# Kernel tuning notes

Measured on AMD Instinct MI355X. Metric: run time of the kernel, lower is better.

Reference implementation:

```python
import jax, jax.numpy as jnp
import numpy as np

H = 4096        # hidden_size
NH = 32         # num attention heads
HD = 128        # head_dim
NKV = 8         # num kv heads
NREP = NH // NKV
THETA = 1e6     # Mixtral rope_theta
EPS = 1e-5      # rmsnorm eps
NBITS = 4       # kv cache quant bits
GROUP = 128     # kv cache quant group size (== head_dim)


def rms_norm(x, w, eps=EPS):
    var = jnp.mean(x * x, axis=-1, keepdims=True)
    return x * jax.lax.rsqrt(var + eps) * w


def fake_int8_per_token(x):
    # symmetric per-row (per-token) int8 quant-dequant: models QLinear.prepare_input
    s = jnp.maximum(jnp.max(jnp.abs(x), axis=-1, keepdims=True) / 127.0, 1e-8)
    return jnp.clip(jnp.round(x / s), -127, 127) * s


def fake_int8_per_channel(w):
    # symmetric per-output-channel int8 quant-dequant of weight [out, in]
    s = jnp.maximum(jnp.max(jnp.abs(w), axis=-1, keepdims=True) / 127.0, 1e-8)
    return jnp.clip(jnp.round(w / s), -127, 127) * s


def qlinear(x_q, w):
    # x_q already fake-quantized activation; w quantized per-channel
    return jnp.einsum('td,od->to', x_q, fake_int8_per_channel(w))


def quantize_int_group(x, nbits=NBITS, group=GROUP):
    # asymmetric min-max group quant-dequant along last dim
    shp = x.shape
    xg = x.reshape(shp[:-1] + (shp[-1] // group, group))
    mn = jnp.min(xg, axis=-1, keepdims=True)
    mx = jnp.max(xg, axis=-1, keepdims=True)
    scale = jnp.maximum((mx - mn) / (2 ** nbits - 1), 1e-8)
    q = jnp.clip(jnp.round((xg - mn) / scale), 0, 2 ** nbits - 1)
    return (q * scale + mn).reshape(shp)


def rotate_half(x):
    x1, x2 = jnp.split(x, 2, axis=-1)
    return jnp.concatenate((-x2, x1), axis=-1)


def rope_tables(seq_len, dim=HD, theta=THETA):
    inv_freq = 1.0 / (theta ** (jnp.arange(0, dim, 2, dtype=jnp.float32) / dim))
    freqs = jnp.arange(seq_len, dtype=jnp.float32)[:, None] * inv_freq[None, :]
    emb = jnp.concatenate((freqs, freqs), axis=-1)  # [S, HD]
    return jnp.cos(emb), jnp.sin(emb)


def setup_inputs() -> dict:
    key = jax.random.key(0)
    ks = jax.random.split(key, 7)
    B, S = 1, 2048
    return {
        'hidden_states': jax.random.normal(ks[0], (B, S, H), dtype=jnp.float32),
        'position_ids': jnp.broadcast_to(jnp.arange(S, dtype=jnp.int32)[None, :], (B, S)),
        'rmsnorm_weight': jax.random.uniform(ks[1], (H,), dtype=jnp.float32, minval=0.5, maxval=1.5),
        'Wq': jax.random.normal(ks[2], (H, H), dtype=jnp.float32) * 0.02,
        'Wk': jax.random.normal(ks[3], (NKV * HD, H), dtype=jnp.float32) * 0.02,
        'Wv': jax.random.normal(ks[4], (NKV * HD, H), dtype=jnp.float32) * 0.02,
        'Wo': jax.random.normal(ks[5], (H, H), dtype=jnp.float32) * 0.02,
    }


def reference(hidden_states, position_ids, rmsnorm_weight, Wq, Wk, Wv, Wo):
    B, S, _ = hidden_states.shape
    x2d = hidden_states.reshape(B * S, H)

    # fused RMSNorm + activation quant (SHARQ prepare_input_rmsnorm)
    xq = fake_int8_per_token(rms_norm(x2d, rmsnorm_weight))

    q = qlinear(xq, Wq).reshape(B, S, NH, HD).transpose(0, 2, 1, 3)    # [B,NH,S,HD]
    k = qlinear(xq, Wk).reshape(B, S, NKV, HD).transpose(0, 2, 1, 3)   # [B,NKV,S,HD]
    v = qlinear(xq, Wv).reshape(B, S, NKV, HD).transpose(0, 2, 1, 3)

    # int4 group quant of K before RoPE (q_kv_cache=True path)
    k = quantize_int_group(k)

    cos_t, sin_t = rope_tables(S)
    cos = cos_t[position_ids][:, None, :, :]   # [B,1,S,HD]
    sin = sin_t[position_ids][:, None, :, :]
    q = q * cos + rotate_half(q) * sin
    k = k * cos + rotate_half(k) * sin

    # GQA repeat (each kv head repeated NREP times consecutively)
    k = jnp.repeat(k, NREP, axis=1)
    v = jnp.repeat(v, NREP, axis=1)

    # int4 group quant of V after repeat (as in source ordering)
    v = quantize_int_group(v)

    # causal SDPA
    scores = jnp.einsum('bhqd,bhkd->bhqk', q, k) / jnp.sqrt(jnp.float32(HD))
    causal = jnp.tril(jnp.ones((S, S), dtype=bool))
    scores = jnp.where(causal[None, None], scores, jnp.float32(-1e9))
    attn = jax.nn.softmax(scores, axis=-1)
    out = jnp.einsum('bhqk,bhkd->bhqd', attn, v)
    out = out.transpose(0, 2, 1, 3).reshape(B * S, H)

    # o_proj with activation quant
    out = qlinear(fake_int8_per_token(out), Wo)
    return out.reshape(B, S, H)
```

## Files before the change

### kernel.cpp

```cpp
#include <hip/hip_runtime.h>


#define SQ   2048
#define HID  4096
#define NHEAD 32
#define HDIM 128
#define NKVH 8
#define KVD  1024
#define QKVN 6144

typedef __attribute__((ext_vector_type(8))) short          bh8;
typedef __attribute__((ext_vector_type(8))) unsigned short us8;
typedef __attribute__((ext_vector_type(4))) float          f4v;
typedef __attribute__((ext_vector_type(4))) int            i32x4;

__device__ __forceinline__ unsigned short f2bf(float f) {
    unsigned u = __float_as_uint(f);
    u += 0x7fffu + ((u >> 16) & 1u);
    return (unsigned short)(u >> 16);
}

__device__ __forceinline__ unsigned cvtpk_bf16(float a, float b) {
    unsigned r;
    asm("v_cvt_pk_bf16_f32 %0, %1, %2" : "=v"(r) : "v"(a), "v"(b));
    return r;
}

__device__ __forceinline__ void gl2lds16(const void* g, void* l) {
    __builtin_amdgcn_global_load_lds(
        (const __attribute__((address_space(1))) unsigned int*)g,
        (__attribute__((address_space(3))) unsigned int*)l, 16, 0, 0);
}

template<int N> __device__ __forceinline__ void vmc() {
    if constexpr (N == 0) asm volatile("s_waitcnt vmcnt(0)" ::: "memory");
    else if constexpr (N == 2) asm volatile("s_waitcnt vmcnt(2)" ::: "memory");
    else if constexpr (N == 4) asm volatile("s_waitcnt vmcnt(4)" ::: "memory");
    else if constexpr (N == 6) asm volatile("s_waitcnt vmcnt(6)" ::: "memory");
    else if constexpr (N == 8) asm volatile("s_waitcnt vmcnt(8)" ::: "memory");
}

__device__ __forceinline__ void rq_body(float v[16],
                                        char* __restrict__ dst,
                                        float* __restrict__ sout,
                                        float* red, int tid, int l, int wv)
{
    float am = 0.f;
#pragma unroll
    for (int i = 0; i < 16; i++) am = fmaxf(am, fabsf(v[i]));
#pragma unroll
    for (int o = 32; o >= 1; o >>= 1) am = fmaxf(am, __shfl_xor(am, o));
    if (l == 0) red[wv] = am;
    __syncthreads();
    am = fmaxf(fmaxf(red[0], red[1]), fmaxf(red[2], red[3]));
    float s = fmaxf(am / 127.0f, 1e-8f);
    float inv = 1.0f / s;
    if (tid == 0) *sout = s;
#pragma unroll
    for (int i = 0; i < 4; i++) {
        unsigned pk = 0;
#pragma unroll
        for (int j = 0; j < 4; j++) {
            float q = rintf(v[4*i+j] * inv);
            q = fminf(fmaxf(q, -127.f), 127.f);
            pk |= ((unsigned)((int)q & 0xff)) << (8 * j);
        }
        ((unsigned*)dst)[i * 256 + tid] = pk;
    }
}

__global__ __launch_bounds__(256) void prequant(
    const float* __restrict__ Wq, const float* __restrict__ Wk,
    const float* __restrict__ Wv, const float* __restrict__ Wo,
    const float* __restrict__ X, const float* __restrict__ rw,
    char* __restrict__ wqkv, char* __restrict__ woq, char* __restrict__ xq,
    float* __restrict__ swqkv, float* __restrict__ swo, float* __restrict__ sx)
{
    int row = blockIdx.x;
    int tid = threadIdx.x;
    int l = tid & 63, wv = tid >> 6;
    const float* src; char* dst; float* sout; bool dorms = false;
    if (row < HID)            { src = Wq + (size_t)row * HID;                 dst = wqkv + (size_t)row * HID; sout = swqkv + row; }
    else if (row < HID + KVD) { src = Wk + (size_t)(row - HID) * HID;         dst = wqkv + (size_t)row * HID; sout = swqkv + row; }
    else if (row < QKVN)      { src = Wv + (size_t)(row - HID - KVD) * HID;   dst = wqkv + (size_t)row * HID; sout = swqkv + row; }
    else if (row < QKVN+HID)  { int r = row - QKVN; src = Wo + (size_t)r * HID; dst = woq + (size_t)r * HID;  sout = swo + r; }
    else { int r = row - QKVN - HID; src = X + (size_t)r * HID; dst = xq + (size_t)r * HID; sout = sx + r; dorms = true; }
    float v[16];
#pragma unroll
    for (int i = 0; i < 4; i++) {
        float4 f = ((const float4*)src)[i * 256 + tid];
        v[4*i+0] = f.x; v[4*i+1] = f.y; v[4*i+2] = f.z; v[4*i+3] = f.w;
    }
    __shared__ float red[4];
    if (dorms) {
        float ss = 0.f;
#pragma unroll
        for (int i = 0; i < 16; i++) ss += v[i] * v[i];
#pragma unroll
        for (int o = 32; o >= 1; o >>= 1) ss += __shfl_xor(ss, o);
        if (l == 0) red[wv] = ss;
        __syncthreads();
        float tot = red[0] + red[1] + red[2] + red[3];
        float rs = rsqrtf(tot * (1.0f / 4096.0f) + 1e-5f);
        __syncthreads();
#pragma unroll
        for (int i = 0; i < 4; i++) {
            float4 wf = ((const float4*)rw)[i * 256 + tid];
            v[4*i+0] = v[4*i+0] * rs * wf.x;
            v[4*i+1] = v[4*i+1] * rs * wf.y;
            v[4*i+2] = v[4*i+2] * rs * wf.z;
            v[4*i+3] = v[4*i+3] * rs * wf.w;
        }
    }
    rq_body(v, dst, sout, red, tid, l, wv);
}

__global__ __launch_bounds__(256) void rowquant_kernel(
    const float* __restrict__ X, char* __restrict__ Q, float* __restrict__ Sout)
{
    int row = blockIdx.x;
    int tid = threadIdx.x;
    int l = tid & 63, wv = tid >> 6;
    const float* xr = X + (size_t)row * 4096;
    float v[16];
#pragma unroll
    for (int i = 0; i < 4; i++) {
        float4 f = ((const float4*)xr)[i * 256 + tid];
        v[4*i+0] = f.x; v[4*i+1] = f.y; v[4*i+2] = f.z; v[4*i+3] = f.w;
    }
    __shared__ float red[4];
    rq_body(v, Q + (size_t)row * 4096, Sout + row, red, tid, l, wv);
}

template<int BN>
__global__ __launch_bounds__(512, 1) void gemm128i8(
    const char* __restrict__ A, const char* __restrict__ B,
    const float* __restrict__ sa, const float* __restrict__ sb,
    float* __restrict__ C, int M, int N, int K, int NBM)
{
    constexpr int NQ  = BN / 128;
    constexpr int BSZ = BN * 128;
    __shared__ char As[2 * 16384];
    __shared__ char Bs[2 * BSZ];
    int tid = threadIdx.x;
    int l = tid & 63, wid = tid >> 6;
    int wr = wid >> 2, wc = wid & 3;
    int g = l >> 4, c = l & 15;
    int wg = blockIdx.x;
    int cpx = (int)gridDim.x >> 3;
    int swz = (wg & 7) * cpx + (wg >> 3);
    int bm = swz % NBM, bn = swz / NBM;
    const char* Ab = A + (size_t)bm * 128 * K;
    const char* Bb = B + (size_t)bn * BN * K;

    auto stageA = [&](int buf, int tt) {
#pragma unroll
        for (int r = 0; r < 2; r++) {
            int e = (r * 512 + tid) * 16;
            int row = e >> 7, chunk = (e >> 4) & 7;
            gl2lds16(Ab + (size_t)row * K + tt * 128 + ((chunk ^ (row & 7)) << 4),
                     As + buf * 16384 + e);
        }
    };
    auto stageB = [&](int buf, int u, int tt) {
#pragma unroll
        for (int r = 0; r < 2; r++) {
            int e = (r * 512 + tid) * 16;
            int row = e >> 7, chunk = (e >> 4) & 7;
            gl2lds16(Bb + (size_t)(u * 128 + row) * K + tt * 128 + ((chunk ^ (row & 7)) << 4),
                     Bs + buf * BSZ + u * 16384 + e);
        }
    };
    i32x4 af[4][2];
    auto LDA = [&](int buf) {
#pragma unroll
        for (int fm = 0; fm < 4; fm++)
#pragma unroll
            for (int kk = 0; kk < 2; kk++) {
                int row = wr * 64 + fm * 16 + c;
                af[fm][kk] = *(const i32x4*)(As + buf * 16384 + row * 128 +
                                             (((kk * 4 + g) ^ (row & 7)) << 4));
            }
    };

    stageA(0, 0);
#pragma unroll
    for (int u = 0; u < NQ; u++) stageB(0, u, 0);

    i32x4 acc[4][2 * NQ] = {};
    int nt = K >> 7;
    for (int t = 0; t < nt; t++) {
        int buf = t & 1;
        bool last = (t == nt - 1);
#pragma unroll
        for (int nq = 0; nq < NQ; nq++) {
            if (last) { if (nq == 0) vmc<0>(); }
            else if (nq == 0) vmc<2 * (NQ - 1)>();
            else vmc<2 * NQ>();
            asm volatile("s_barrier" ::: "memory");
            if (!last) {
                if (nq == 0) { stageA(buf ^ 1, t + 1); stageB(buf ^ 1, 0, t + 1); }
                else stageB(buf ^ 1, nq, t + 1);
            }
            if (nq == 0) LDA(buf);
            i32x4 bf[2][2];
#pragma unroll
            for (int fn = 0; fn < 2; fn++)
#pragma unroll
                for (int kk = 0; kk < 2; kk++) {
                    int rowu = wc * 32 + fn * 16 + c;
                    bf[fn][kk] = *(const i32x4*)(Bs + buf * BSZ + nq * 16384 +
                                                 rowu * 128 +
                                                 (((kk * 4 + g) ^ (rowu & 7)) << 4));
                }
            asm volatile("s_waitcnt lgkmcnt(0)" ::: "memory");
            __builtin_amdgcn_sched_barrier(0);
            __builtin_amdgcn_s_setprio(1);
#pragma unroll
            for (int kk = 0; kk < 2; kk++)
#pragma unroll
                for (int fm = 0; fm < 4; fm++)
#pragma unroll
                    for (int fn = 0; fn < 2; fn++)
                        acc[fm][nq * 2 + fn] = __builtin_amdgcn_mfma_i32_16x16x64_i8(
                            af[fm][kk], bf[fn][kk], acc[fm][nq * 2 + fn], 0, 0, 0);
            __builtin_amdgcn_s_setprio(0);
        }
    }
#pragma unroll
    for (int fm = 0; fm < 4; fm++)
#pragma unroll
        for (int j = 0; j < 4; j++) {
            int row = bm * 128 + wr * 64 + fm * 16 + g * 4 + j;
            float sr = sa[row];
#pragma unroll
            for (int q = 0; q < 2 * NQ; q++) {
                int col = bn * BN + (q >> 1) * 128 + wc * 32 + (q & 1) * 16 + c;
                C[(size_t)row * N + col] = (float)acc[fm][q][j] * sr * sb[col];
            }
        }
}

__global__ __launch_bounds__(256) void postq(
    const float* __restrict__ QKVf, const int* __restrict__ pos,
    unsigned short* __restrict__ Qbo, unsigned short* __restrict__ Kbo,
    unsigned short* __restrict__ Vbt)
{
    __shared__ unsigned short T[64][136];
    int bid = blockIdx.x;
    if (bid < 256) {
        int t0 = (bid & 31) * 64;
        int kvh = bid >> 5;
        int tid = threadIdx.x;
        int r = tid >> 2, q4 = tid & 3;
        const float* gp = QKVf + (size_t)(t0 + r) * QKVN + (HID + KVD) + kvh * 128 + q4 * 32;
        float v[32];
#pragma unroll
        for (int i = 0; i < 8; i++) {
            float4 f = ((const float4*)gp)[i];
            v[4*i+0] = f.x; v[4*i+1] = f.y; v[4*i+2] = f.z; v[4*i+3] = f.w;
        }
        float mn = v[0], mx = v[0];
#pragma unroll
        for (int i = 1; i < 32; i++) { mn = fminf(mn, v[i]); mx = fmaxf(mx, v[i]); }
        mn = fminf(mn, __shfl_xor(mn, 1)); mx = fmaxf(mx, __shfl_xor(mx, 1));
        mn = fminf(mn, __shfl_xor(mn, 2)); mx = fmaxf(mx, __shfl_xor(mx, 2));
        float sc = fmaxf((mx - mn) / 15.0f, 1e-8f);
#pragma unroll
        for (int i = 0; i < 32; i++) {
            float q = fminf(fmaxf(rintf((v[i] - mn) / sc), 0.f), 15.f);
            T[r][q4 * 32 + i] = f2bf(q * sc + mn);
        }
        __syncthreads();
        int d = tid >> 1, hf = tid & 1;
#pragma unroll
        for (int b = 0; b < 4; b++) {
            us8 o;
#pragma unroll
            for (int j = 0; j < 8; j++) o[j] = T[hf * 32 + b * 8 + j][d];
            *(us8*)(Vbt + (size_t)(kvh * 128 + d) * SQ + t0 + hf * 32 + b * 8) = o;
        }
        return;
    }
    int wid = (bid - 256) * 4 + (threadIdx.x >> 6);
    int l = threadIdx.x & 63;
    float fr = exp2f(-(float)l * 0.3114307588956902f);
    if (wid < SQ * NKVH) {
        int t = wid >> 3, kvh = wid & 7;
        const float* gp = QKVf + (size_t)t * QKVN + HID + kvh * 128;
        float x1 = gp[l], x2 = gp[l + 64];
        float mn = fminf(x1, x2), mx = fmaxf(x1, x2);
#pragma unroll
        for (int o = 32; o >= 1; o >>= 1) {
            mn = fminf(mn, __shfl_xor(mn, o));
            mx = fmaxf(mx, __shfl_xor(mx, o));
        }
        float sc = fmaxf((mx - mn) / 15.0f, 1e-8f);
        float q1 = fminf(fmaxf(rintf((x1 - mn) / sc), 0.f), 15.f);
        float q2 = fminf(fmaxf(rintf((x2 - mn) / sc), 0.f), 15.f);
        x1 = q1 * sc + mn;
        x2 = q2 * sc + mn;
        float ang = (float)pos[t] * fr;
        float cs = cosf(ang), sn = sinf(ang);
        unsigned short* op = Kbo + (size_t)t * KVD + kvh * 128;
        op[l]      = f2bf(x1 * cs - x2 * sn);
        op[l + 64] = f2bf(x2 * cs + x1 * sn);
    } else {
        const float QSCL = (float)(0.08838834764831845 * 1.4426950408889634);
        int w2 = wid - SQ * NKVH;
        int t = w2 >> 5, h = w2 & 31;
        const float* gp = QKVf + (size_t)t * QKVN + h * 128;
        float x1 = gp[l], x2 = gp[l + 64];
        float ang = (float)pos[t] * fr;
        float cs = cosf(ang), sn = sinf(ang);
        unsigned short* op = Qbo + (size_t)t * HID + h * 128;
        op[l]      = f2bf((x1 * cs - x2 * sn) * QSCL);
        op[l + 64] = f2bf((x2 * cs + x1 * sn) * QSCL);
    }
}

__global__ __launch_bounds__(256, 2) void attn_kernel(
    const unsigned short* __restrict__ Qb, const unsigned short* __restrict__ Kb,
    const unsigned short* __restrict__ Vbt, float* __restrict__ AO)
{
    int j = blockIdx.x;
    int h = blockIdx.y;
    int kvh = h >> 2;
    int tid = threadIdx.x;
    int l = tid & 63, w = tid >> 6;
    int g = l >> 4, c = l & 15;
    __shared__ unsigned short Ks[2 * 8192];
    __shared__ unsigned short Vt[128 * 64];
    __shared__ unsigned short Plds[4][2][16][72];
    int rowA = j * 64 + w * 16 + c;
    int rowB = (31 - j) * 64 + w * 16 + c;
    int NT = 32 - j;

    auto stageK = [&](int buf, int kv0) {
#pragma unroll
        for (int i = 0; i < 4; i++) {
            int e = (i * 256 + tid) * 8;
            int row = e >> 7, chunk = (e >> 3) & 15;
            gl2lds16(Kb + (size_t)(kv0 + row) * KVD + kvh * 128 + ((chunk ^ (row & 15)) << 3),
                     Ks + buf * 8192 + e);
        }
    };
    us8 vreg[4];
    auto stageV = [&](int kv0) {
#pragma unroll
        for (int i = 0; i < 4; i++) {
            int e = (i * 256 + tid) * 8;
            int r = e >> 6, cc = e & 63;
            vreg[i] = *(const us8*)(Vbt + (size_t)(kvh * 128 + r) * SQ + kv0 + cc);
        }
    };
    auto writeV = [&]() {
#pragma unroll
        for (int i = 0; i < 4; i++) {
            int e = (i * 256 + tid) * 8;
            int rv = e >> 6, chv = (e >> 3) & 7;
            *(us8*)(Vt + rv * 64 + ((chv ^ (rv & 7)) << 3)) = vreg[i];
        }
    };
    auto softmax = [&](f4v (&sf)[4], float& mrun, float& lrun, f4v (&acc)[8],
                       unsigned short* PW) {
        float pmax = sf[0][0];
#pragma unroll
        for (int n = 0; n < 4; n++)
#pragma unroll
            for (int jj = 0; jj < 4; jj++) pmax = fmaxf(pmax, sf[n][jj]);
        pmax = fmaxf(pmax, __shfl_xor(pmax, 16));
        pmax = fmaxf(pmax, __shfl_xor(pmax, 32));
        if (__any(pmax - mrun > 8.0f)) {
            float mnew = fmaxf(mrun, pmax);
            float alpha = exp2f(mrun - mnew);
            mrun = mnew;
            lrun *= alpha;
#pragma unroll
            for (int n = 0; n < 8; n++) acc[n] *= alpha;
        }
        float rsum = 0.f;
#pragma unroll
        for (int n = 0; n < 4; n++)
#pragma unroll
            for (int jj = 0; jj < 4; jj++) {
                float pv = exp2f(sf[n][jj] - mrun);
                sf[n][jj] = pv;
                rsum += pv;
            }
        rsum += __shfl_xor(rsum, 16);
        rsum += __shfl_xor(rsum, 32);
        lrun += rsum;
#pragma unroll
        for (int n = 0; n < 4; n++) {
            uint2 u;
            u.x = cvtpk_bf16(sf[n][0], sf[n][1]);
            u.y = cvtpk_bf16(sf[n][2], sf[n][3]);
            *(uint2*)(PW + c * 72 + n * 16 + g * 4) = u;
        }
    };

    stageK(0, 0);
    stageV(0);

    bh8 qfA[4], qfB[4];
    {
        const unsigned short* qa = Qb + (size_t)rowA * HID + h * 128;
        const unsigned short* qp = Qb + (size_t)rowB * HID + h * 128;
#pragma unroll
        for (int kk = 0; kk < 4; kk++) {
            qfA[kk] = *(const bh8*)(qa + kk * 32 + g * 8);
            qfB[kk] = *(const bh8*)(qp + kk * 32 + g * 8);
        }
    }
    writeV();
    asm volatile("s_waitcnt vmcnt(0)" ::: "memory");
    __syncthreads();

    float mrunB = -1e30f, lrunB = 0.f;
    f4v accB[8] = {};

    {
        float mrunA = -1e30f, lrunA = 0.f;
        f4v accA[8] = {};
        for (int t = 0; t <= j; t++) {
            int kv0 = t * 64;
            int buf = t & 1;
            stageK(buf ^ 1, kv0 + 64);
            stageV(kv0 + 64);
            f4v sfA[4], sfB[4];
            __builtin_amdgcn_s_setprio(1);
#pragma unroll
            for (int n = 0; n < 4; n++) {
                f4v aA = {}, aB = {};
                int rowk = n * 16 + c;
#pragma unroll
                for (int kk = 0; kk < 4; kk++) {
                    bh8 kf = *(const bh8*)(Ks + buf * 8192 + rowk * 128 +
                                           (((kk * 4 + g) ^ (rowk & 15)) << 3));
                    aA = __builtin_amdgcn_mfma_f32_16x16x32_bf16(kf, qfA[kk], aA, 0, 0, 0);
                    aB = __builtin_amdgcn_mfma_f32_16x16x32_bf16(kf, qfB[kk], aB, 0, 0, 0);
                }
                sfA[n] = aA; sfB[n] = aB;
            }
            __builtin_amdgcn_s_setprio(0);
            if (t == j) {
#pragma unroll
                for (int n = 0; n < 4; n++)
#pragma unroll
                    for (int jj = 0; jj < 4; jj++)
                        if (kv0 + n * 16 + g * 4 + jj > rowA) sfA[n][jj] = -1e30f;
            }
            softmax(sfA, mrunA, lrunA, accA, &Plds[w][0][0][0]);
            softmax(sfB, mrunB, lrunB, accB, &Plds[w][1][0][0]);
            __builtin_amdgcn_s_setprio(1);
#pragma unroll
            for (int kk = 0; kk < 2; kk++) {
                bh8 pbA = *(const bh8*)(&Plds[w][0][c][kk * 32 + g * 8]);
                bh8 pbB = *(const bh8*)(&Plds[w][1][c][kk * 32 + g * 8]);
#pragma unroll
                for (int n = 0; n < 8; n++) {
                    int rowv = n * 16 + c;
                    bh8 vf = *(const bh8*)(Vt + rowv * 64 + (((kk * 4 + g) ^ (rowv & 7)) << 3));
                    accA[n] = __builtin_amdgcn_mfma_f32_16x16x32_bf16(vf, pbA, accA[n], 0, 0, 0);
                    accB[n] = __builtin_amdgcn_mfma_f32_16x16x32_bf16(vf, pbB, accB[n], 0, 0, 0);
                }
            }
            __builtin_amdgcn_s_setprio(0);
            __syncthreads();
            writeV();
            asm volatile("s_waitcnt vmcnt(0)" ::: "memory");
            __syncthreads();
        }
        float invA = 1.0f / lrunA;
#pragma unroll
        for (int n = 0; n < 8; n++) {
            f4v oA = accA[n] * invA;
            *(f4v*)(AO + (size_t)rowA * HID + h * 128 + n * 16 + g * 4) = oA;
        }
    }

    for (int t = j + 1; t < NT; t++) {
        int kv0 = t * 64;
        int buf = t & 1;
        if (t + 1 < NT) { stageK(buf ^ 1, kv0 + 64); stageV(kv0 + 64); }
        f4v sfB[4];
        __builtin_amdgcn_s_setprio(1);
#pragma unroll
        for (int n = 0; n < 4; n++) {
            f4v aB = {};
            int rowk = n * 16 + c;
#pragma unroll
            for (int kk = 0; kk < 4; kk++) {
                bh8 kf = *(const bh8*)(Ks + buf * 8192 + rowk * 128 +
                                       (((kk * 4 + g) ^ (rowk & 15)) << 3));
                aB = __builtin_amdgcn_mfma_f32_16x16x32_bf16(kf, qfB[kk], aB, 0, 0, 0);
            }
            sfB[n] = aB;
        }
        __builtin_amdgcn_s_setprio(0);
        if (t == NT - 1) {
#pragma unroll
            for (int n = 0; n < 4; n++)
#pragma unroll
                for (int jj = 0; jj < 4; jj++)
                    if (kv0 + n * 16 + g * 4 + jj > rowB) sfB[n][jj] = -1e30f;
        }
        softmax(sfB, mrunB, lrunB, accB, &Plds[w][1][0][0]);
        __builtin_amdgcn_s_setprio(1);
#pragma unroll
        for (int kk = 0; kk < 2; kk++) {
            bh8 pbB = *(const bh8*)(&Plds[w][1][c][kk * 32 + g * 8]);
#pragma unroll
            for (int n = 0; n < 8; n++) {
                int rowv = n * 16 + c;
                bh8 vf = *(const bh8*)(Vt + rowv * 64 + (((kk * 4 + g) ^ (rowv & 7)) << 3));
                accB[n] = __builtin_amdgcn_mfma_f32_16x16x32_bf16(vf, pbB, accB[n], 0, 0, 0);
            }
        }
        __builtin_amdgcn_s_setprio(0);
        if (t + 1 < NT) {
            __syncthreads();
            writeV();
            asm volatile("s_waitcnt vmcnt(0)" ::: "memory");
            __syncthreads();
        }
    }
    float invB = 1.0f / lrunB;
#pragma unroll
    for (int n = 0; n < 8; n++) {
        f4v oB = accB[n] * invB;
        *(f4v*)(AO + (size_t)rowB * HID + h * 128 + n * 16 + g * 4) = oB;
    }
}

extern "C" void kernel_launch(void* const* d_in, const int* in_sizes, int n_in,
                              void* d_out, int out_size, void* d_ws, size_t ws_size,
                              hipStream_t stream)
{
    const float* x   = (const float*)d_in[0];
    const int*   pos = (const int*)d_in[1];
    const float* rw  = (const float*)d_in[2];
    const float* Wq  = (const float*)d_in[3];
    const float* Wk  = (const float*)d_in[4];
    const float* Wv  = (const float*)d_in[5];
    const float* Wo  = (const float*)d_in[6];
    float* out = (float*)d_out;

    char* p = (char*)d_ws;
    auto alloc = [&](size_t bytes) -> void* {
        void* r = (void*)p;
        p += (bytes + 255) & ~(size_t)255;
        return r;
    };
    char*           xq    = (char*)alloc((size_t)SQ * HID);
    float*          sx    = (float*)alloc(SQ * 4);
    char*           wqkv  = (char*)alloc((size_t)QKVN * HID);
    char*           woq   = (char*)alloc((size_t)HID * HID);
    float*          swqkv = (float*)alloc(QKVN * 4);
    float*          swo   = (float*)alloc(HID * 4);
    float*          QKVf  = (float*)alloc((size_t)SQ * QKVN * 4);
    unsigned short* Qb    = (unsigned short*)alloc((size_t)SQ * HID * 2);
    unsigned short* Kb    = (unsigned short*)alloc((size_t)SQ * KVD * 2);
    unsigned short* Vbt   = (unsigned short*)alloc((size_t)SQ * KVD * 2);
    float*          sa    = (float*)alloc(SQ * 4);

    size_t need = (size_t)(p - (char*)d_ws);
    if (ws_size < need) {
        hipMemsetAsync(d_out, 0x7f, 4, stream);
        return;
    }
    float*          AO   = QKVf;
    char*           attq = (char*)(QKVf + (size_t)SQ * HID);
    prequant<<<QKVN + HID + SQ, 256, 0, stream>>>(
        Wq, Wk, Wv, Wo, x, rw, wqkv, woq, xq, swqkv, swo, sx);
    gemm128i8<384><<<dim3((SQ / 128) * (QKVN / 384)), 512, 0, stream>>>(
        xq, wqkv, sx, swqkv, QKVf, SQ, QKVN, HID, SQ / 128);
    postq<<<256 + (SQ * NKVH + SQ * NHEAD) / 4, 256, 0, stream>>>(
        QKVf, pos, Qb, Kb, Vbt);
    attn_kernel<<<dim3(16, NHEAD), 256, 0, stream>>>(Qb, Kb, Vbt, AO);
    rowquant_kernel<<<SQ, 256, 0, stream>>>(AO, attq, sa);
    gemm128i8<256><<<dim3((SQ / 128) * (HID / 256)), 512, 0, stream>>>(
        attq, woq, sa, swo, out, SQ, HID, HID, SQ / 128);
}
```

Baseline: 243.2 us.

## Double-buffer V in LDS via direct global-to-LDS loads, share one P buffer

```diff
diff --git a/kernel.cpp b/kernel.cpp
--- a/kernel.cpp
+++ b/kernel.cpp
@@ -330,11 +330,12 @@
     int l = tid & 63, w = tid >> 6;
     int g = l >> 4, c = l & 15;
     __shared__ unsigned short Ks[2 * 8192];
-    __shared__ unsigned short Vt[128 * 64];
-    __shared__ unsigned short Plds[4][2][16][72];
+    __shared__ unsigned short Vs[2 * 8192];
+    __shared__ unsigned short Plds[4][16][72];
     int rowA = j * 64 + w * 16 + c;
     int rowB = (31 - j) * 64 + w * 16 + c;
     int NT = 32 - j;
+    unsigned short* pw = &Plds[w][0][0];
 
     auto stageK = [&](int buf, int kv0) {
 #pragma unroll
@@ -345,25 +346,16 @@
                      Ks + buf * 8192 + e);
         }
     };
-    us8 vreg[4];
-    auto stageV = [&](int kv0) {
-#pragma unroll
-        for (int i = 0; i < 4; i++) {
-            int e = (i * 256 + tid) * 8;
-            int r = e >> 6, cc = e & 63;
-            vreg[i] = *(const us8*)(Vbt + (size_t)(kvh * 128 + r) * SQ + kv0 + cc);
-        }
-    };
-    auto writeV = [&]() {
+    auto stageV = [&](int buf, int kv0) {
 #pragma unroll
         for (int i = 0; i < 4; i++) {
             int e = (i * 256 + tid) * 8;
             int rv = e >> 6, chv = (e >> 3) & 7;
-            *(us8*)(Vt + rv * 64 + ((chv ^ (rv & 7)) << 3)) = vreg[i];
-        }
-    };
-    auto softmax = [&](f4v (&sf)[4], float& mrun, float& lrun, f4v (&acc)[8],
-                       unsigned short* PW) {
+            gl2lds16(Vbt + (size_t)(kvh * 128 + rv) * SQ + kv0 + ((chv ^ (rv & 7)) << 3),
+                     Vs + buf * 8192 + e);
+        }
+    };
+    auto softmax = [&](f4v (&sf)[4], float& mrun, float& lrun, f4v (&acc)[8]) {
         float pmax = sf[0][0];
 #pragma unroll
         for (int n = 0; n < 4; n++)
@@ -396,12 +388,16 @@
             uint2 u;
             u.x = cvtpk_bf16(sf[n][0], sf[n][1]);
             u.y = cvtpk_bf16(sf[n][2], sf[n][3]);
-            *(uint2*)(PW + c * 72 + n * 16 + g * 4) = u;
-        }
+            *(uint2*)(pw + c * 72 + n * 16 + g * 4) = u;
+        }
+    };
+    auto loadP = [&](bh8 (&pb)[2]) {
+        pb[0] = *(const bh8*)(pw + c * 72 + g * 8);
+        pb[1] = *(const bh8*)(pw + c * 72 + 32 + g * 8);
     };
 
     stageK(0, 0);
-    stageV(0);
+    stageV(0, 0);
 
     bh8 qfA[4], qfB[4];
     {
@@ -413,8 +409,7 @@
             qfB[kk] = *(const bh8*)(qp + kk * 32 + g * 8);
         }
     }
-    writeV();
-    asm volatile("s_waitcnt vmcnt(0)" ::: "memory");
+    vmc<0>();
     __syncthreads();
 
     float mrunB = -1e30f, lrunB = 0.f;
@@ -427,7 +422,7 @@
             int kv0 = t * 64;
             int buf = t & 1;
             stageK(buf ^ 1, kv0 + 64);
-            stageV(kv0 + 64);
+            stageV(buf ^ 1, kv0 + 64);
             f4v sfA[4], sfB[4];
             __builtin_amdgcn_s_setprio(1);
 #pragma unroll
@@ -451,25 +446,25 @@
                     for (int jj = 0; jj < 4; jj++)
                         if (kv0 + n * 16 + g * 4 + jj > rowA) sfA[n][jj] = -1e30f;
             }
-            softmax(sfA, mrunA, lrunA, accA, &Plds[w][0][0][0]);
-            softmax(sfB, mrunB, lrunB, accB, &Plds[w][1][0][0]);
+            bh8 pbA[2], pbB[2];
+            softmax(sfA, mrunA, lrunA, accA);
+            loadP(pbA);
+            softmax(sfB, mrunB, lrunB, accB);
+            loadP(pbB);
             __builtin_amdgcn_s_setprio(1);
 #pragma unroll
             for (int kk = 0; kk < 2; kk++) {
-                bh8 pbA = *(const bh8*)(&Plds[w][0][c][kk * 32 + g * 8]);
-                bh8 pbB = *(const bh8*)(&Plds[w][1][c][kk * 32 + g * 8]);
 #pragma unroll
                 for (int n = 0; n < 8; n++) {
                     int rowv = n * 16 + c;
-                    bh8 vf = *(const bh8*)(Vt + rowv * 64 + (((kk * 4 + g) ^ (rowv & 7)) << 3));
-                    accA[n] = __builtin_amdgcn_mfma_f32_16x16x32_bf16(vf, pbA, accA[n], 0, 0, 0);
-                    accB[n] = __builtin_amdgcn_mfma_f32_16x16x32_bf16(vf, pbB, accB[n], 0, 0, 0);
+                    bh8 vf = *(const bh8*)(Vs + buf * 8192 + rowv * 64 +
+                                           (((kk * 4 + g) ^ (rowv & 7)) << 3));
+                    accA[n] = __builtin_amdgcn_mfma_f32_16x16x32_bf16(vf, pbA[kk], accA[n], 0, 0, 0);
+                    accB[n] = __builtin_amdgcn_mfma_f32_16x16x32_bf16(vf, pbB[kk], accB[n], 0, 0, 0);
                 }
             }
             __builtin_amdgcn_s_setprio(0);
-            __syncthreads();
-            writeV();
-            asm volatile("s_waitcnt vmcnt(0)" ::: "memory");
+            vmc<0>();
             __syncthreads();
         }
         float invA = 1.0f / lrunA;
@@ -483,7 +478,7 @@
     for (int t = j + 1; t < NT; t++) {
         int kv0 = t * 64;
         int buf = t & 1;
-        if (t + 1 < NT) { stageK(buf ^ 1, kv0 + 64); stageV(kv0 + 64); }
+        if (t + 1 < NT) { stageK(buf ^ 1, kv0 + 64); stageV(buf ^ 1, kv0 + 64); }
         f4v sfB[4];
         __builtin_amdgcn_s_setprio(1);
 #pragma unroll
@@ -506,23 +501,23 @@
                 for (int jj = 0; jj < 4; jj++)
                     if (kv0 + n * 16 + g * 4 + jj > rowB) sfB[n][jj] = -1e30f;
         }
-        softmax(sfB, mrunB, lrunB, accB, &Plds[w][1][0][0]);
+        bh8 pbB[2];
+        softmax(sfB, mrunB, lrunB, accB);
+        loadP(pbB);
         __builtin_amdgcn_s_setprio(1);
 #pragma unroll
         for (int kk = 0; kk < 2; kk++) {
-            bh8 pbB = *(const bh8*)(&Plds[w][1][c][kk * 32 + g * 8]);
 #pragma unroll
             for (int n = 0; n < 8; n++) {
                 int rowv = n * 16 + c;
-                bh8 vf = *(const bh8*)(Vt + rowv * 64 + (((kk * 4 + g) ^ (rowv & 7)) << 3));
-                accB[n] = __builtin_amdgcn_mfma_f32_16x16x32_bf16(vf, pbB, accB[n], 0, 0, 0);
+                bh8 vf = *(const bh8*)(Vs + buf * 8192 + rowv * 64 +
+                                       (((kk * 4 + g) ^ (rowv & 7)) << 3));
+                accB[n] = __builtin_amdgcn_mfma_f32_16x16x32_bf16(vf, pbB[kk], accB[n], 0, 0, 0);
             }
         }
         __builtin_amdgcn_s_setprio(0);
         if (t + 1 < NT) {
-            __syncthreads();
-            writeV();
-            asm volatile("s_waitcnt vmcnt(0)" ::: "memory");
+            vmc<0>();
             __syncthreads();
         }
     }
```

After: 242.8 us. No clear change (-0.2%).
